# Performance work log

Hardware: AMD Instinct MI355X
Metric: run time of the kernel (lower is better)

Reference implementation:

```python
import jax, jax.numpy as jnp
import numpy as np

B, S, L, H, D, DF = 2, 1024, 2, 8, 512, 2048
DK = D // H  # head dim (dk == dv == 64)
EPS = 1e-5


def _ln(x, g, b):
    m = jnp.mean(x, axis=-1, keepdims=True)
    v = jnp.mean((x - m) ** 2, axis=-1, keepdims=True)
    return (x - m) / jnp.sqrt(v + EPS) * g + b


def setup_inputs() -> dict:
    key = jax.random.key(0)
    ks = jax.random.split(key, 8)
    sd = 1.0 / np.sqrt(D)
    sf = 1.0 / np.sqrt(DF)
    inp = {
        "src": jax.random.normal(ks[0], (B, S, D), jnp.float32),
        "Wq": jax.random.normal(ks[1], (L, D, D), jnp.float32) * sd,
        "bq": jnp.zeros((L, D), jnp.float32),
        "Wk": jax.random.normal(ks[2], (L, D, D), jnp.float32) * sd,
        "bk": jnp.zeros((L, D), jnp.float32),
        "Wv": jax.random.normal(ks[3], (L, D, D), jnp.float32) * sd,
        "bv": jnp.zeros((L, D), jnp.float32),
        "Wo": jax.random.normal(ks[4], (L, D, D), jnp.float32) * sd,
        "bo": jnp.zeros((L, D), jnp.float32),
        "W1": jax.random.normal(ks[5], (L, D, DF), jnp.float32) * sd,
        "b1": jnp.zeros((L, DF), jnp.float32),
        "W2": jax.random.normal(ks[6], (L, DF, D), jnp.float32) * sf,
        "b2": jnp.zeros((L, D), jnp.float32),
        "g1": jnp.ones((L, D), jnp.float32),
        "be1": jnp.zeros((L, D), jnp.float32),
        "g2": jnp.ones((L, D), jnp.float32),
        "be2": jnp.zeros((L, D), jnp.float32),
        "gf": jnp.ones((D,), jnp.float32),
        "bef": jnp.zeros((D,), jnp.float32),
    }
    return inp


def _heads(x):
    # [B,S,D] -> [B,H,S,DK]
    return x.reshape(B, S, H, DK).transpose(0, 2, 1, 3)


def _causal_linear_attention(q, k, v):
    # Faithful to torch: cumsum of per-step KV outer products, then query contraction.
    kv = jnp.einsum("bhsk,bhsv->bhskv", k, v)      # [B,H,S,DK,DK]
    cum = jnp.cumsum(kv, axis=2)                     # prefix sums over sequence
    return jnp.einsum("bhsk,bhskv->bhsv", q, cum)   # [B,H,S,DK]


def reference(src, Wq, bq, Wk, bk, Wv, bv, Wo, bo, W1, b1, W2, b2,
              g1, be1, g2, be2, gf, bef):
    x = src
    for i in range(L):
        q = _heads(x @ Wq[i] + bq[i])
        k = _heads(x @ Wk[i] + bk[i])
        v = _heads(x @ Wv[i] + bv[i])
        att = _causal_linear_attention(q, k, v)
        att = att.transpose(0, 2, 1, 3).reshape(B, S, D)
        att = att @ Wo[i] + bo[i]
        x = _ln(x + att, g1[i], be1[i])              # post-norm (normalize_before=False)
        ff = jax.nn.relu(x @ W1[i] + b1[i]) @ W2[i] + b2[i]
        x = _ln(x + ff, g2[i], be2[i])
    return _ln(x, gf, bef)                            # final encoder LayerNorm
```

## Files before the change

kernel.cpp:

```cpp
#include <hip/hip_runtime.h>
#include <hip/hip_bf16.h>

#define DEV static __device__ __forceinline__

typedef __attribute__((ext_vector_type(8))) short short8;
typedef __attribute__((ext_vector_type(4))) float f32x4;

DEV unsigned short f2b(float f){
  unsigned int u = __float_as_uint(f);
  return (unsigned short)((u + 0x7FFFu + ((u >> 16) & 1u)) >> 16);
}
DEV float b2f(unsigned short h){ return __uint_as_float(((unsigned int)h) << 16); }
DEV float load_in(const void* p, size_t i, int isbf){
  return isbf ? b2f(((const unsigned short*)p)[i]) : ((const float*)p)[i];
}
DEV void load_lds16(const unsigned short* g, unsigned short* l){
  __builtin_amdgcn_global_load_lds(
      (const __attribute__((address_space(1))) void*)g,
      (__attribute__((address_space(3))) void*)l, 16, 0, 0);
}

DEV int detect_isbf_block(const void* src){
  __shared__ int cnt[4];
  int tid = threadIdx.x;
  float v = b2f(((const unsigned short*)src)[2 * tid]);
  float av = fabsf(v);
  bool sane = ((av < 64.0f) && (av > 9.5e-7f)) || (v == 0.0f);
  unsigned long long m = __ballot(sane);
  if ((tid & 63) == 0) cnt[tid >> 6] = __popcll(m);
  __syncthreads();
  int tot = cnt[0] + cnt[1] + cnt[2] + cnt[3];
  __syncthreads();
  return tot > 128;
}

struct WDesc { const void* src; long src_off; unsigned short* dst; int K; int N; int tstart; };
struct WParams { WDesc d[12]; const void* dsrc; };

__global__ __launch_bounds__(256) void ingest_weights(WParams P){
  __shared__ float tile[32][33];
  int isbf = detect_isbf_block(P.dsrc);
  int b = blockIdx.x;
  int t = 0;
  #pragma unroll
  for (int i = 1; i < 12; ++i) if (b >= P.d[i].tstart) t = i;
  WDesc d = P.d[t];
  int r = b - d.tstart;
  int tiles_x = d.N >> 5;
  int tx = r % tiles_x, ty = r / tiles_x;
  int lx = threadIdx.x & 31, ly = threadIdx.x >> 5;
  #pragma unroll
  for (int i = 0; i < 4; ++i){
    int row = ty*32 + ly + i*8;
    int col = tx*32 + lx;
    tile[ly + i*8][lx] = load_in(d.src, (size_t)d.src_off + (size_t)row*d.N + col, isbf);
  }
  __syncthreads();
  #pragma unroll
  for (int i = 0; i < 4; ++i){
    int orow = tx*32 + ly + i*8;
    int ocol = ty*32 + lx;
    d.dst[(size_t)orow*d.K + ocol] = f2b(tile[lx][ly + i*8]);
  }
}

struct SDesc { const void* src; int src_off; int dstart; };
struct SParams { SDesc d[22]; float* dst; int total; };

__global__ __launch_bounds__(256) void ingest_misc(SParams S, const void* src,
                                                   float* xf, unsigned short* xb){
  int isbf = detect_isbf_block(src);
  int b = blockIdx.x, tid = threadIdx.x;
  if (b < 4096){
    int i = b*256 + tid;
    float v = load_in(src, (size_t)i, isbf);
    xf[i] = v; xb[i] = f2b(v);
  } else {
    int i = (b - 4096)*256 + tid;
    if (i < S.total){
      int t = 0;
      #pragma unroll
      for (int j = 1; j < 22; ++j) if (i >= S.d[j].dstart) t = j;
      S.dst[i] = load_in(S.d[t].src, (size_t)S.d[t].src_off + (i - S.d[t].dstart), isbf);
    }
  }
}

struct GemmArgs {
  const unsigned short* A;
  const unsigned short* Bt;
  const float* bias;
  float* Cf;
  unsigned short* Cb;
  int K;
  int lda, ldb, ldc;
  int cshift, cmask;
  size_t cstride;
  size_t cfz;
  int relu;
};

template<int BN>
__global__ __launch_bounds__(256) void gemm_bt(GemmArgs g){
  constexpr int NI = (BN == 128) ? 4 : 2;
  constexpr int NJ = 4;
  __shared__ __align__(16) unsigned short sA[128*32];
  __shared__ __align__(16) unsigned short sB[BN*32];
  int tid = threadIdx.x;
  int koff = blockIdx.z * g.K;
  int K = g.K, lda = g.lda, ldb = g.ldb;
  size_t bm = (size_t)blockIdx.y * 128, bn = (size_t)blockIdx.x * BN;
  int lane = tid & 63, wv = tid >> 6, quad = lane >> 4, l16 = lane & 15;
  int wm = (BN == 128) ? (wv >> 1) * 64 : wv * 32;
  int wn = (BN == 128) ? (wv & 1) * 64 : 0;
  f32x4 acc[NI][NJ];
  #pragma unroll
  for (int i=0;i<NI;++i)
    #pragma unroll
    for (int j=0;j<NJ;++j) acc[i][j] = (f32x4){0.f,0.f,0.f,0.f};
  const unsigned short* Ap = g.A  + (bm + (tid>>2))*lda + koff + (tid&3)*8;
  const unsigned short* Bp = g.Bt + (bn + (tid>>2))*ldb + koff + (tid&3)*8;
  for (int ko = 0; ko < K; ko += 32){
    __syncthreads();
    load_lds16(Ap + ko,                  &sA[tid*8]);
    load_lds16(Ap + (size_t)64*lda + ko, &sA[2048 + tid*8]);
    load_lds16(Bp + ko,                  &sB[tid*8]);
    if (BN == 128)
      load_lds16(Bp + (size_t)64*ldb + ko, &sB[2048 + tid*8]);
    __syncthreads();
    short8 af[NI], bfv[NJ];
    #pragma unroll
    for (int i=0;i<NI;++i) af[i]  = *(const short8*)&sA[(wm + i*16 + l16)*32 + quad*8];
    #pragma unroll
    for (int j=0;j<NJ;++j) bfv[j] = *(const short8*)&sB[(wn + j*16 + l16)*32 + quad*8];
    #pragma unroll
    for (int i=0;i<NI;++i)
      #pragma unroll
      for (int j=0;j<NJ;++j)
        acc[i][j] = __builtin_amdgcn_mfma_f32_16x16x32_bf16(af[i], bfv[j], acc[i][j], 0,0,0);
  }
  float* Cf = g.Cf ? g.Cf + (size_t)blockIdx.z * g.cfz : nullptr;
  unsigned short* Cb = g.Cb;
  #pragma unroll
  for (int j=0;j<NJ;++j){
    int col = (int)bn + wn + j*16 + l16;
    float bv = g.bias ? g.bias[col] : 0.f;
    size_t cbase = ((size_t)(col >> g.cshift))*g.cstride + (col & g.cmask);
    #pragma unroll
    for (int i=0;i<NI;++i){
      #pragma unroll
      for (int r=0;r<4;++r){
        int row = (int)bm + wm + i*16 + quad*4 + r;
        float v = acc[i][j][r] + bv;
        if (g.relu) v = fmaxf(v, 0.f);
        size_t idx = cbase + (size_t)row*g.ldc;
        if (Cf) Cf[idx] = v;
        if (Cb) Cb[idx] = f2b(v);
      }
    }
  }
}

#define ATT_S 1024
#define ATT_D 512

__global__ __launch_bounds__(256) void attn_state_kernel(
    const unsigned short* k, const unsigned short* v, float* states)
{
  __shared__ __align__(16) unsigned short sVt[64*72];
  __shared__ __align__(16) unsigned short sKt[64*72];
  int tid = threadIdx.x;
  int c = blockIdx.x, bh = blockIdx.y;
  int b = bh >> 3, h = bh & 7;
  const size_t base = ((size_t)b*ATT_S + (size_t)c*64)*ATT_D + h*64;
  int lane = tid & 63, wv = tid >> 6, quad = lane >> 4, l16 = lane & 15;

  int t = lane, vc = wv*8;
  const unsigned short* vp = v + base + (size_t)t*ATT_D;
  const unsigned short* kp = k + base + (size_t)t*ATT_D;
  float4 v0 = *(const float4*)(vp + vc);
  float4 v1 = *(const float4*)(vp + vc + 32);
  float4 k0 = *(const float4*)(kp + vc);
  float4 k1 = *(const float4*)(kp + vc + 32);
  {
    const unsigned short* pv0 = (const unsigned short*)&v0;
    const unsigned short* pv1 = (const unsigned short*)&v1;
    const unsigned short* pk0 = (const unsigned short*)&k0;
    const unsigned short* pk1 = (const unsigned short*)&k1;
    #pragma unroll
    for (int e = 0; e < 8; ++e){
      sVt[(vc+e)*72 + t]    = pv0[e];
      sVt[(vc+32+e)*72 + t] = pv1[e];
      sKt[(vc+e)*72 + t]    = pk0[e];
      sKt[(vc+32+e)*72 + t] = pk1[e];
    }
  }
  __syncthreads();

  f32x4 acc[4];
  #pragma unroll
  for (int j=0;j<4;++j) acc[j] = (f32x4){0.f,0.f,0.f,0.f};
  #pragma unroll
  for (int kk=0;kk<2;++kk){
    short8 a = *(const short8*)&sVt[(wv*16 + l16)*72 + kk*32 + quad*8];
    #pragma unroll
    for (int j=0;j<4;++j){
      short8 bb = *(const short8*)&sKt[(j*16 + l16)*72 + kk*32 + quad*8];
      acc[j] = __builtin_amdgcn_mfma_f32_16x16x32_bf16(a, bb, acc[j], 0,0,0);
    }
  }
  float* st = states + ((size_t)bh*16 + c)*4096;
  #pragma unroll
  for (int j=0;j<4;++j)
    #pragma unroll
    for (int rr=0;rr<4;++rr)
      st[(wv*16 + quad*4 + rr)*64 + j*16 + l16] = acc[j][rr];
}

__global__ __launch_bounds__(256) void attn_out_kernel(
    const unsigned short* q, const unsigned short* k, const unsigned short* v,
    const float* states, unsigned short* att)
{
  __shared__ __align__(16) unsigned short sQ [64*72];
  __shared__ __align__(16) unsigned short sK [64*72];
  __shared__ __align__(16) unsigned short sVt[64*72];
  __shared__ __align__(16) float sKV[64*68];
  int tid = threadIdx.x;
  int c = blockIdx.x, bh = blockIdx.y;
  int b = bh >> 3, h = bh & 7;
  const size_t base = ((size_t)b*ATT_S + (size_t)c*64)*ATT_D + h*64;
  int lane = tid & 63, wv = tid >> 6, quad = lane >> 4, l16 = lane & 15;

  float4 racc[4];
  #pragma unroll
  for (int u=0;u<4;++u) racc[u] = (float4){0.f,0.f,0.f,0.f};
  const float* sbase = states + (size_t)bh*16*4096;
  for (int cc = 0; cc < c; ++cc){
    const float4* sp = (const float4*)(sbase + (size_t)cc*4096);
    #pragma unroll
    for (int u=0;u<4;++u){
      float4 t4 = sp[tid + u*256];
      racc[u].x += t4.x; racc[u].y += t4.y; racc[u].z += t4.z; racc[u].w += t4.w;
    }
  }
  #pragma unroll
  for (int u=0;u<4;++u){
    int e = (tid + u*256)*4;
    int row = e >> 6, col = e & 63;
    *(float4*)&sKV[row*68 + col] = racc[u];
  }

  int r = tid >> 2, c8 = (tid & 3)*8;
  const unsigned short* qp = q + base + (size_t)r*ATT_D;
  const unsigned short* kp = k + base + (size_t)r*ATT_D;
  float4 q0 = *(const float4*)(qp + c8);
  float4 q1 = *(const float4*)(qp + c8 + 32);
  float4 k0 = *(const float4*)(kp + c8);
  float4 k1 = *(const float4*)(kp + c8 + 32);
  int t = lane, vc = wv*8;
  const unsigned short* vp = v + base + (size_t)t*ATT_D;
  float4 v0 = *(const float4*)(vp + vc);
  float4 v1 = *(const float4*)(vp + vc + 32);
  *(float4*)&sQ[r*72 + c8]      = q0;
  *(float4*)&sQ[r*72 + c8 + 32] = q1;
  *(float4*)&sK[r*72 + c8]      = k0;
  *(float4*)&sK[r*72 + c8 + 32] = k1;
  {
    const unsigned short* pv0 = (const unsigned short*)&v0;
    const unsigned short* pv1 = (const unsigned short*)&v1;
    #pragma unroll
    for (int e=0;e<8;++e){
      sVt[(vc+e)*72 + t]    = pv0[e];
      sVt[(vc+32+e)*72 + t] = pv1[e];
    }
  }
  __syncthreads();

  f32x4 accS[4];
  #pragma unroll
  for (int j=0;j<4;++j) accS[j] = (f32x4){0.f,0.f,0.f,0.f};
  #pragma unroll
  for (int kk=0;kk<2;++kk){
    short8 a = *(const short8*)&sQ[(wv*16 + l16)*72 + kk*32 + quad*8];
    #pragma unroll
    for (int j=0;j<4;++j){
      short8 bb = *(const short8*)&sK[(j*16 + l16)*72 + kk*32 + quad*8];
      accS[j] = __builtin_amdgcn_mfma_f32_16x16x32_bf16(a, bb, accS[j], 0,0,0);
    }
  }
  __syncthreads();

  #pragma unroll
  for (int j=0;j<4;++j)
    #pragma unroll
    for (int rr=0;rr<4;++rr){
      int i  = wv*16 + quad*4 + rr;
      int cj = j*16 + l16;
      sK[i*72 + cj] = f2b((i >= cj) ? accS[j][rr] : 0.f);
    }

  f32x4 accO[4];
  #pragma unroll
  for (int j=0;j<4;++j) accO[j] = (f32x4){0.f,0.f,0.f,0.f};
  #pragma unroll
  for (int kk=0;kk<2;++kk){
    short8 a = *(const short8*)&sQ[(wv*16 + l16)*72 + kk*32 + quad*8];
    #pragma unroll
    for (int j=0;j<4;++j){
      const float* pf = &sKV[(j*16 + l16)*68 + kk*32 + quad*8];
      short8 bb;
      #pragma unroll
      for (int e=0;e<8;++e) ((unsigned short*)&bb)[e] = f2b(pf[e]);
      accO[j] = __builtin_amdgcn_mfma_f32_16x16x32_bf16(a, bb, accO[j], 0,0,0);
    }
  }
  __syncthreads();

  #pragma unroll
  for (int kk=0;kk<2;++kk){
    short8 a = *(const short8*)&sK[(wv*16 + l16)*72 + kk*32 + quad*8];
    #pragma unroll
    for (int j=0;j<4;++j){
      short8 bb = *(const short8*)&sVt[(j*16 + l16)*72 + kk*32 + quad*8];
      accO[j] = __builtin_amdgcn_mfma_f32_16x16x32_bf16(a, bb, accO[j], 0,0,0);
    }
  }
  #pragma unroll
  for (int j=0;j<4;++j)
    #pragma unroll
    for (int rr=0;rr<4;++rr){
      int i  = wv*16 + quad*4 + rr;
      int cj = j*16 + l16;
      att[base + (size_t)i*ATT_D + cj] = f2b(accO[j][rr]);
    }
}

__global__ __launch_bounds__(256) void add_ln_kernel(
    const float* x, const float* p, int np, const float* bias,
    const float* g, const float* bta,
    float* outf, unsigned short* outb, void* outd, const void* dsrc, int rows)
{
  int isbf = 0;
  if (dsrc) isbf = detect_isbf_block(dsrc);
  int row = blockIdx.x*4 + (threadIdx.x >> 6);
  int lane = threadIdx.x & 63;
  if (row >= rows) return;
  const float* xr = x + (size_t)row*512;
  float a[8];
  *(float4*)&a[0] = *(const float4*)(xr + lane*4);
  *(float4*)&a[4] = *(const float4*)(xr + 256 + lane*4);
  for (int s = 0; s < np; ++s){
    const float* pr = p + (size_t)s*1048576 + (size_t)row*512;
    float yb[8];
    *(float4*)&yb[0] = *(const float4*)(pr + lane*4);
    *(float4*)&yb[4] = *(const float4*)(pr + 256 + lane*4);
    #pragma unroll
    for (int e=0;e<8;++e) a[e] += yb[e];
  }
  if (bias){
    float bb2[8];
    *(float4*)&bb2[0] = *(const float4*)(bias + lane*4);
    *(float4*)&bb2[4] = *(const float4*)(bias + 256 + lane*4);
    #pragma unroll
    for (int e=0;e<8;++e) a[e] += bb2[e];
  }
  float s = 0.f, qq = 0.f;
  #pragma unroll
  for (int e=0;e<8;++e){ s += a[e]; qq += a[e]*a[e]; }
  #pragma unroll
  for (int off=32; off>0; off>>=1){
    s  += __shfl_xor(s,  off, 64);
    qq += __shfl_xor(qq, off, 64);
  }
  float mean = s * (1.f/512.f);
  float var  = qq * (1.f/512.f) - mean*mean;
  float rstd = rsqrtf(var + 1e-5f);
  float gg[8], bb[8];
  *(float4*)&gg[0] = *(const float4*)(g + lane*4);
  *(float4*)&gg[4] = *(const float4*)(g + 256 + lane*4);
  *(float4*)&bb[0] = *(const float4*)(bta + lane*4);
  *(float4*)&bb[4] = *(const float4*)(bta + 256 + lane*4);
  #pragma unroll
  for (int e=0;e<8;++e) a[e] = (a[e]-mean)*rstd*gg[e] + bb[e];
  if (outf){
    float* orow = outf + (size_t)row*512;
    *(float4*)(orow + lane*4)       = *(float4*)&a[0];
    *(float4*)(orow + 256 + lane*4) = *(float4*)&a[4];
  }
  if (outb){
    unsigned short* orow = outb + (size_t)row*512;
    #pragma unroll
    for (int e=0;e<4;++e){ orow[lane*4+e] = f2b(a[e]); orow[256+lane*4+e] = f2b(a[4+e]); }
  }
  if (outd){
    if (isbf){
      unsigned short* od = (unsigned short*)outd + (size_t)row*512;
      #pragma unroll
      for (int e=0;e<4;++e){ od[lane*4+e] = f2b(a[e]); od[256+lane*4+e] = f2b(a[4+e]); }
    } else {
      float* od = (float*)outd + (size_t)row*512;
      *(float4*)(od + lane*4)       = *(float4*)&a[0];
      *(float4*)(od + 256 + lane*4) = *(float4*)&a[4];
    }
  }
}

extern "C" void kernel_launch(void* const* d_in, const int* in_sizes, int n_in,
                              void* d_out, int out_size, void* d_ws, size_t ws_size,
                              hipStream_t stream)
{
  (void)in_sizes; (void)n_in; (void)out_size; (void)ws_size;
  const void* src = d_in[0];
  const void* Wq = d_in[1];  const void* bq = d_in[2];
  const void* Wk = d_in[3];  const void* bk = d_in[4];
  const void* Wv = d_in[5];  const void* bv = d_in[6];
  const void* Wo = d_in[7];  const void* bo = d_in[8];
  const void* W1 = d_in[9];  const void* b1 = d_in[10];
  const void* W2 = d_in[11]; const void* b2 = d_in[12];
  const void* g1 = d_in[13]; const void* be1 = d_in[14];
  const void* g2 = d_in[15]; const void* be2 = d_in[16];
  const void* gf = d_in[17]; const void* bef = d_in[18];

  char* W = (char*)d_ws;
  float* smalls          = (float*)(W + 256);
  unsigned short* wt     = (unsigned short*)(W + 65536);
  float* x_f             = (float*)(W + 12648448);
  unsigned short* x_b    = (unsigned short*)(W + 16842752);
  unsigned short* q_b    = (unsigned short*)(W + 18939904);
  unsigned short* att_b  = (unsigned short*)(W + 25231360);
  float* pp              = (float*)(W + 27328512);
  unsigned short* h1_b   = (unsigned short*)(W + 44105728);
  float* states          = (float*)(W + 44105728);
  unsigned short* k_b = q_b + 1048576;
  unsigned short* v_b = q_b + 2097152;

  WParams wp;
  {
    const void* wsrc[6] = {Wq, Wk, Wv, Wo, W1, W2};
    int wK[6] = {512,512,512,512,512,2048};
    int wN[6] = {512,512,512,512,2048,512};
    long wsz[6] = {262144,262144,262144,262144,1048576,1048576};
    int tstart = 0; size_t dsto = 0;
    for (int l=0;l<2;++l)
      for (int ti=0;ti<6;++ti){
        int idx = l*6+ti;
        wp.d[idx].src = wsrc[ti];
        wp.d[idx].src_off = (long)l * wsz[ti];
        wp.d[idx].dst = wt + dsto;
        wp.d[idx].K = wK[ti]; wp.d[idx].N = wN[ti];
        wp.d[idx].tstart = tstart;
        tstart += (wK[ti]/32)*(wN[ti]/32);
        dsto += (size_t)wsz[ti];
      }
    wp.dsrc = src;
    ingest_weights<<<dim3(6144), 256, 0, stream>>>(wp);
  }

  SParams sp;
  {
    const void* ss[10] = {bq,bk,bv,bo,b1,b2,g1,be1,g2,be2};
    int slen[10] = {512,512,512,512,2048,512,512,512,512,512};
    int dcur = 0, di = 0;
    for (int l=0;l<2;++l)
      for (int ti=0;ti<10;++ti){
        sp.d[di].src = ss[ti];
        sp.d[di].src_off = l * slen[ti];
        sp.d[di].dstart = dcur;
        dcur += slen[ti]; ++di;
      }
    sp.d[20].src = gf;  sp.d[20].src_off = 0; sp.d[20].dstart = dcur; dcur += 512;
    sp.d[21].src = bef; sp.d[21].src_off = 0; sp.d[21].dstart = dcur; dcur += 512;
    sp.dst = smalls; sp.total = dcur;
    ingest_misc<<<dim3(4152), 256, 0, stream>>>(sp, src, x_f, x_b);
  }

  for (int l = 0; l < 2; ++l){
    unsigned short* WqkvT = wt + (size_t)l*3145728;
    unsigned short* WoT   = WqkvT + 786432;
    unsigned short* W1T   = WqkvT + 1048576;
    unsigned short* W2T   = WqkvT + 2097152;
    float* base  = smalls + l*6656;
    float* p_bqkv= base;
    float* p_bo  = base + 1536;
    float* p_b1  = base + 2048;
    float* p_b2  = base + 4096;
    float* p_g1  = base + 4608;
    float* p_be1 = base + 5120;
    float* p_g2  = base + 5632;
    float* p_be2 = base + 6144;

    GemmArgs qkv = {};
    qkv.A = x_b; qkv.Bt = WqkvT; qkv.bias = p_bqkv;
    qkv.Cf = nullptr; qkv.Cb = q_b;
    qkv.K = 512; qkv.lda = 512; qkv.ldb = 512; qkv.ldc = 512;
    qkv.cshift = 9; qkv.cmask = 511; qkv.cstride = 1048576; qkv.cfz = 0; qkv.relu = 0;
    gemm_bt<64><<<dim3(24,16,1), 256, 0, stream>>>(qkv);

    attn_state_kernel<<<dim3(16,16), 256, 0, stream>>>(k_b, v_b, states);
    attn_out_kernel<<<dim3(16,16), 256, 0, stream>>>(q_b, k_b, v_b, states, att_b);

    GemmArgs go = {};
    go.A = att_b; go.Bt = WoT; go.bias = nullptr;
    go.Cf = pp; go.Cb = nullptr;
    go.K = 256; go.lda = 512; go.ldb = 512; go.ldc = 512;
    go.cshift = 30; go.cmask = 0x3fffffff; go.cstride = 0; go.cfz = 1048576; go.relu = 0;
    gemm_bt<64><<<dim3(8,16,2), 256, 0, stream>>>(go);

    add_ln_kernel<<<dim3(512), 256, 0, stream>>>(x_f, pp, 2, p_bo, p_g1, p_be1,
                                                 x_f, x_b, nullptr, nullptr, 2048);

    GemmArgs f1 = {};
    f1.A = x_b; f1.Bt = W1T; f1.bias = p_b1;
    f1.Cf = nullptr; f1.Cb = h1_b;
    f1.K = 512; f1.lda = 512; f1.ldb = 512; f1.ldc = 2048;
    f1.cshift = 30; f1.cmask = 0x3fffffff; f1.cstride = 0; f1.cfz = 0; f1.relu = 1;
    gemm_bt<128><<<dim3(16,16,1), 256, 0, stream>>>(f1);

    GemmArgs f2 = {};
    f2.A = h1_b; f2.Bt = W2T; f2.bias = nullptr;
    f2.Cf = pp; f2.Cb = nullptr;
    f2.K = 512; f2.lda = 2048; f2.ldb = 2048; f2.ldc = 512;
    f2.cshift = 30; f2.cmask = 0x3fffffff; f2.cstride = 0; f2.cfz = 1048576; f2.relu = 0;
    gemm_bt<64><<<dim3(8,16,4), 256, 0, stream>>>(f2);

    add_ln_kernel<<<dim3(512), 256, 0, stream>>>(x_f, pp, 4, p_b2, p_g2, p_be2,
                                                 x_f, x_b, nullptr, nullptr, 2048);
  }

  add_ln_kernel<<<dim3(512), 256, 0, stream>>>(x_f, nullptr, 0, nullptr,
                                               smalls + 13312, smalls + 13824,
                                               nullptr, nullptr, d_out, src, 2048);
}
```

Measured before the change: 278.1 us.

## Double GEMM K-tile to 64 with XOR-swizzled LDS layout

The bf16 MFMA GEMM now stages a 64-wide K slice per iteration instead of 32, halving the number of barrier pairs per K loop. It also XOR-swizzles the 16-byte chunks in LDS by row so that fragment reads avoid bank conflicts. In exchange, LDS usage per block doubles, which can lower occupancy, and each K dimension must be a multiple of 64.

```diff
diff --git a/kernel.cpp b/kernel.cpp
--- a/kernel.cpp
+++ b/kernel.cpp
@@ -104,8 +104,9 @@
 __global__ __launch_bounds__(256) void gemm_bt(GemmArgs g){
   constexpr int NI = (BN == 128) ? 4 : 2;
   constexpr int NJ = 4;
-  __shared__ __align__(16) unsigned short sA[128*32];
-  __shared__ __align__(16) unsigned short sB[BN*32];
+  constexpr int BPASS = BN / 32;
+  __shared__ __align__(16) unsigned short sA[128*64];
+  __shared__ __align__(16) unsigned short sB[BN*64];
   int tid = threadIdx.x;
   int koff = blockIdx.z * g.K;
   int K = g.K, lda = g.lda, ldb = g.ldb;
@@ -118,26 +119,40 @@
   for (int i=0;i<NI;++i)
     #pragma unroll
     for (int j=0;j<NJ;++j) acc[i][j] = (f32x4){0.f,0.f,0.f,0.f};
-  const unsigned short* Ap = g.A  + (bm + (tid>>2))*lda + koff + (tid&3)*8;
-  const unsigned short* Bp = g.Bt + (bn + (tid>>2))*ldb + koff + (tid&3)*8;
-  for (int ko = 0; ko < K; ko += 32){
+  int srow = tid >> 3;
+  int schunk = (tid & 7) ^ (srow & 7);
+  const unsigned short* Ap = g.A  + (bm + srow)*lda + koff + schunk*8;
+  const unsigned short* Bp = g.Bt + (bn + srow)*ldb + koff + schunk*8;
+  for (int ko = 0; ko < K; ko += 64){
     __syncthreads();
-    load_lds16(Ap + ko,                  &sA[tid*8]);
-    load_lds16(Ap + (size_t)64*lda + ko, &sA[2048 + tid*8]);
-    load_lds16(Bp + ko,                  &sB[tid*8]);
-    if (BN == 128)
-      load_lds16(Bp + (size_t)64*ldb + ko, &sB[2048 + tid*8]);
+    #pragma unroll
+    for (int p = 0; p < 4; ++p)
+      load_lds16(Ap + (size_t)(p*32)*lda + ko, &sA[p*2048 + tid*8]);
+    #pragma unroll
+    for (int p = 0; p < BPASS; ++p)
+      load_lds16(Bp + (size_t)(p*32)*ldb + ko, &sB[p*2048 + tid*8]);
     __syncthreads();
-    short8 af[NI], bfv[NJ];
-    #pragma unroll
-    for (int i=0;i<NI;++i) af[i]  = *(const short8*)&sA[(wm + i*16 + l16)*32 + quad*8];
-    #pragma unroll
-    for (int j=0;j<NJ;++j) bfv[j] = *(const short8*)&sB[(wn + j*16 + l16)*32 + quad*8];
-    #pragma unroll
-    for (int i=0;i<NI;++i)
-      #pragma unroll
-      for (int j=0;j<NJ;++j)
-        acc[i][j] = __builtin_amdgcn_mfma_f32_16x16x32_bf16(af[i], bfv[j], acc[i][j], 0,0,0);
+    #pragma unroll
+    for (int kk = 0; kk < 2; ++kk){
+      short8 af[NI], bfv[NJ];
+      #pragma unroll
+      for (int i=0;i<NI;++i){
+        int row = wm + i*16 + l16;
+        int ch  = (kk*4 + quad) ^ (row & 7);
+        af[i] = *(const short8*)&sA[row*64 + ch*8];
+      }
+      #pragma unroll
+      for (int j=0;j<NJ;++j){
+        int row = wn + j*16 + l16;
+        int ch  = (kk*4 + quad) ^ (row & 7);
+        bfv[j] = *(const short8*)&sB[row*64 + ch*8];
+      }
+      #pragma unroll
+      for (int i=0;i<NI;++i)
+        #pragma unroll
+        for (int j=0;j<NJ;++j)
+          acc[i][j] = __builtin_amdgcn_mfma_f32_16x16x32_bf16(af[i], bfv[j], acc[i][j], 0,0,0);
+    }
   }
   float* Cf = g.Cf ? g.Cf + (size_t)blockIdx.z * g.cfz : nullptr;
   unsigned short* Cb = g.Cb;
```

Result: faster. 267.4 us (-3.8%).
